# Kernel optimization log

Hardware: AMD Instinct MI355X
Metric: run time of the kernel (lower is better)

The kernel has to match this reference:

```python
import jax, jax.numpy as jnp
import numpy as np

# Config matching YoloLayer(anchor_mask=[0,1,2], num_classes=80,
#                           anchors=[116,90,156,198,373,326], num_anchors=3)
B, H, W = 32, 76, 76
NUM_CLASSES = 80
NUM_ANCHORS = 3
ANCHORS = [116.0, 90.0, 156.0, 198.0, 373.0, 326.0]
STRIDE = 32.0
C = (5 + NUM_CLASSES) * NUM_ANCHORS  # 255


def setup_inputs() -> dict:
    key = jax.random.key(0)
    output = jax.random.normal(key, (B, C, H, W), dtype=jnp.float32)
    # conf threshold (self.thresh / nms_thresh in the original forward)
    nms_thresh = jnp.float32(0.6)
    return {"output": output, "nms_thresh": nms_thresh}


def reference(output, nms_thresh):
    """Vectorized, jit-able version of get_region_boxes.

    Instead of Python-loop box lists (data-dependent shape), returns:
      boxes: [B, A, H*W, 7] = (bcx/w, bcy/h, bw/w, bh/h, det_conf,
                               cls_max_conf, cls_max_id)
      keep:  [B, A, H*W] bool mask, det_conf > thresh (only_objectness=1)
    Same math as the original decode + threshold filter.
    """
    b, _, h, w = output.shape
    na, nc = NUM_ANCHORS, NUM_CLASSES
    # masked anchors divided by stride, as in YoloLayer.forward
    anch = jnp.asarray(ANCHORS, dtype=jnp.float32).reshape(na, 2) / STRIDE

    # channel layout is (anchor, 5+nc) per the original view()
    o = output.reshape(b, na, 5 + nc, h * w)  # [B, A, 85, HW]

    # grid offsets flattened in row-major (cy, cx) order, matching ind = cy*w+cx
    gx = jnp.tile(jnp.arange(w, dtype=output.dtype), h)     # [HW]
    gy = jnp.repeat(jnp.arange(h, dtype=output.dtype), w)   # [HW]

    xs = (jax.nn.sigmoid(o[:, :, 0]) + gx) / w               # [B, A, HW]
    ys = (jax.nn.sigmoid(o[:, :, 1]) + gy) / h
    ws = jnp.exp(o[:, :, 2]) * anch[None, :, 0, None] / w
    hs = jnp.exp(o[:, :, 3]) * anch[None, :, 1, None] / h
    det_confs = jax.nn.sigmoid(o[:, :, 4])                   # [B, A, HW]

    cls_confs = jax.nn.softmax(o[:, :, 5:], axis=2)          # [B, A, NC, HW]
    cls_max_confs = jnp.max(cls_confs, axis=2)               # [B, A, HW]
    cls_max_ids = jnp.argmax(cls_confs, axis=2)              # [B, A, HW]

    boxes = jnp.stack(
        [xs, ys, ws, hs, det_confs, cls_max_confs,
         cls_max_ids.astype(output.dtype)],
        axis=-1,
    )  # [B, A, HW, 7]
    keep = det_confs > nms_thresh  # only_objectness=1 path
    return boxes, keep
```

## Files before the change

kernel.cpp:

```cpp
#include <hip/hip_runtime.h>
#include <math.h>


namespace {
constexpr int kB   = 32;
constexpr int kA   = 3;
constexpr int kNC  = 80;
constexpr int kH   = 76;
constexpr int kW   = 76;
constexpr int kHW  = kH * kW;
constexpr int kCPA = 5 + kNC;
constexpr int kTot = kB * kA * kHW;
}

__global__ __launch_bounds__(256)
void yolo_decode_kernel(const float* __restrict__ in,
                        const float* __restrict__ thrp,
                        float* __restrict__ out)
{
    const int t = blockIdx.x * 256 + threadIdx.x;
    if (t >= kTot) return;

    const float thresh = thrp[0];

    const int hw = t % kHW;
    const int ba = t / kHW;
    const int a  = ba % kA;

    const float* __restrict__ base = in + (size_t)ba * kCPA * kHW + (size_t)hw;

    const float x0 = base[0 * kHW];
    const float x1 = base[1 * kHW];
    const float x2 = base[2 * kHW];
    const float x3 = base[3 * kHW];
    const float x4 = base[4 * kHW];

    float c[kNC];
    const float* __restrict__ cbase = base + 5 * kHW;
#pragma unroll
    for (int k = 0; k < kNC; ++k) c[k] = cbase[(size_t)k * kHW];

    float m = c[0];
#pragma unroll
    for (int k = 1; k < kNC; ++k) m = fmaxf(m, c[k]);

    float s    = 0.0f;
    float emax = -1.0f;
    int   id   = 0;
#pragma unroll
    for (int k = 0; k < kNC; ++k) {
        const float e = expf(c[k] - m);
        s += e;
        if (e > emax) { emax = e; id = k; }
    }
    const float cls_conf = emax / s;

    const int gx = hw % kW;
    const int gy = hw / kW;

    const float anchw[kA] = {116.0f / 32.0f, 156.0f / 32.0f, 373.0f / 32.0f};
    const float anchh[kA] = { 90.0f / 32.0f, 198.0f / 32.0f, 326.0f / 32.0f};

    constexpr float invW = 1.0f / (float)kW;
    constexpr float invH = 1.0f / (float)kH;

    const float sig0 = 1.0f / (1.0f + expf(-x0));
    const float sig1 = 1.0f / (1.0f + expf(-x1));
    const float det  = 1.0f / (1.0f + expf(-x4));

    const float xs = (sig0 + (float)gx) * invW;
    const float ys = (sig1 + (float)gy) * invH;
    const float ws = expf(x2) * anchw[a] * invW;
    const float hs = expf(x3) * anchh[a] * invH;

    float* __restrict__ bp = out + (size_t)t * 7;
    bp[0] = xs;
    bp[1] = ys;
    bp[2] = ws;
    bp[3] = hs;
    bp[4] = det;
    bp[5] = cls_conf;
    bp[6] = (float)id;

    out[(size_t)kTot * 7 + t] = (det > thresh) ? 1.0f : 0.0f;
}

extern "C" void kernel_launch(void* const* d_in, const int* in_sizes, int n_in,
                              void* d_out, int out_size, void* d_ws, size_t ws_size,
                              hipStream_t stream) {
    (void)in_sizes; (void)n_in; (void)d_ws; (void)ws_size; (void)out_size;
    const float* in   = (const float*)d_in[0];
    const float* thrp = (const float*)d_in[1];
    float* out        = (float*)d_out;

    constexpr int kBlock = 256;
    constexpr int kGrid  = (kTot + kBlock - 1) / kBlock;
    yolo_decode_kernel<<<kGrid, kBlock, 0, stream>>>(in, thrp, out);
}
```

Measured before the change: 266.1 us.

## Process four pixels per thread with float4 loads/stores and single-pass softmax

```diff
diff --git a/kernel.cpp b/kernel.cpp
--- a/kernel.cpp
+++ b/kernel.cpp
@@ -9,80 +9,104 @@
 constexpr int kH   = 76;
 constexpr int kW   = 76;
 constexpr int kHW  = kH * kW;
+constexpr int kQ   = kHW / 4;
 constexpr int kCPA = 5 + kNC;
 constexpr int kTot = kB * kA * kHW;
+constexpr int kT4  = kB * kA * kQ;
 }
 
+__device__ __forceinline__ float sigm(float x) { return 1.0f / (1.0f + expf(-x)); }
+
 __global__ __launch_bounds__(256)
-void yolo_decode_kernel(const float* __restrict__ in,
-                        const float* __restrict__ thrp,
-                        float* __restrict__ out)
+void yolo_decode4(const float* __restrict__ in,
+                  const float* __restrict__ thrp,
+                  float* __restrict__ out)
 {
     const int t = blockIdx.x * 256 + threadIdx.x;
-    if (t >= kTot) return;
+    if (t >= kT4) return;
 
     const float thresh = thrp[0];
 
-    const int hw = t % kHW;
-    const int ba = t / kHW;
+    const int q  = t % kQ;
+    const int ba = t / kQ;
     const int a  = ba % kA;
 
-    const float* __restrict__ base = in + (size_t)ba * kCPA * kHW + (size_t)hw;
+    const float4* __restrict__ base4 =
+        reinterpret_cast<const float4*>(in + (size_t)ba * kCPA * kHW) + q;
 
-    const float x0 = base[0 * kHW];
-    const float x1 = base[1 * kHW];
-    const float x2 = base[2 * kHW];
-    const float x3 = base[3 * kHW];
-    const float x4 = base[4 * kHW];
+    const float4 cx = base4[0 * kQ];
+    const float4 cy = base4[1 * kQ];
+    const float4 cw = base4[2 * kQ];
+    const float4 ch = base4[3 * kQ];
+    const float4 co = base4[4 * kQ];
 
-    float c[kNC];
-    const float* __restrict__ cbase = base + 5 * kHW;
-#pragma unroll
-    for (int k = 0; k < kNC; ++k) c[k] = cbase[(size_t)k * kHW];
+    float s0 = 0.f, s1 = 0.f, s2 = 0.f, s3 = 0.f;
+    float e0 = -1.f, e1 = -1.f, e2 = -1.f, e3 = -1.f;
+    int   i0 = 0, i1 = 0, i2 = 0, i3 = 0;
+#pragma unroll 10
+    for (int k = 0; k < kNC; ++k) {
+        const float4 c = base4[(size_t)(5 + k) * kQ];
+        const float a0 = expf(c.x);
+        const float a1 = expf(c.y);
+        const float a2 = expf(c.z);
+        const float a3 = expf(c.w);
+        s0 += a0; s1 += a1; s2 += a2; s3 += a3;
+        if (a0 > e0) { e0 = a0; i0 = k; }
+        if (a1 > e1) { e1 = a1; i1 = k; }
+        if (a2 > e2) { e2 = a2; i2 = k; }
+        if (a3 > e3) { e3 = a3; i3 = k; }
+    }
+    const float cc0 = e0 / s0, cc1 = e1 / s1, cc2 = e2 / s2, cc3 = e3 / s3;
 
-    float m = c[0];
-#pragma unroll
-    for (int k = 1; k < kNC; ++k) m = fmaxf(m, c[k]);
+    const int hw  = q * 4;
+    const int gxb = hw % kW;
+    const int gy  = hw / kW;
 
-    float s    = 0.0f;
-    float emax = -1.0f;
-    int   id   = 0;
-#pragma unroll
-    for (int k = 0; k < kNC; ++k) {
-        const float e = expf(c[k] - m);
-        s += e;
-        if (e > emax) { emax = e; id = k; }
-    }
-    const float cls_conf = emax / s;
-
-    const int gx = hw % kW;
-    const int gy = hw / kW;
-
-    const float anchw[kA] = {116.0f / 32.0f, 156.0f / 32.0f, 373.0f / 32.0f};
-    const float anchh[kA] = { 90.0f / 32.0f, 198.0f / 32.0f, 326.0f / 32.0f};
+    const float aw = (a == 0) ? (116.0f / 32.0f) : (a == 1) ? (156.0f / 32.0f) : (373.0f / 32.0f);
+    const float ah = (a == 0) ? ( 90.0f / 32.0f) : (a == 1) ? (198.0f / 32.0f) : (326.0f / 32.0f);
 
     constexpr float invW = 1.0f / (float)kW;
     constexpr float invH = 1.0f / (float)kH;
 
-    const float sig0 = 1.0f / (1.0f + expf(-x0));
-    const float sig1 = 1.0f / (1.0f + expf(-x1));
-    const float det  = 1.0f / (1.0f + expf(-x4));
+    const float ysv = (sigm(cy.x) + (float)gy) * invH;
+    const float ys0 = ysv, ys1 = (sigm(cy.y) + (float)gy) * invH,
+                ys2 = (sigm(cy.z) + (float)gy) * invH,
+                ys3 = (sigm(cy.w) + (float)gy) * invH;
+    (void)ysv;
 
-    const float xs = (sig0 + (float)gx) * invW;
-    const float ys = (sig1 + (float)gy) * invH;
-    const float ws = expf(x2) * anchw[a] * invW;
-    const float hs = expf(x3) * anchh[a] * invH;
+    const float xs0 = (sigm(cx.x) + (float)(gxb + 0)) * invW;
+    const float xs1 = (sigm(cx.y) + (float)(gxb + 1)) * invW;
+    const float xs2 = (sigm(cx.z) + (float)(gxb + 2)) * invW;
+    const float xs3 = (sigm(cx.w) + (float)(gxb + 3)) * invW;
 
-    float* __restrict__ bp = out + (size_t)t * 7;
-    bp[0] = xs;
-    bp[1] = ys;
-    bp[2] = ws;
-    bp[3] = hs;
-    bp[4] = det;
-    bp[5] = cls_conf;
-    bp[6] = (float)id;
+    const float ws0 = expf(cw.x) * aw * invW;
+    const float ws1 = expf(cw.y) * aw * invW;
+    const float ws2 = expf(cw.z) * aw * invW;
+    const float ws3 = expf(cw.w) * aw * invW;
 
-    out[(size_t)kTot * 7 + t] = (det > thresh) ? 1.0f : 0.0f;
+    const float hs0 = expf(ch.x) * ah * invH;
+    const float hs1 = expf(ch.y) * ah * invH;
+    const float hs2 = expf(ch.z) * ah * invH;
+    const float hs3 = expf(ch.w) * ah * invH;
+
+    const float dt0 = sigm(co.x), dt1 = sigm(co.y), dt2 = sigm(co.z), dt3 = sigm(co.w);
+
+    const float id0 = (float)i0, id1 = (float)i1, id2 = (float)i2, id3 = (float)i3;
+
+    float4* __restrict__ bp = reinterpret_cast<float4*>(out + (size_t)t * 28);
+    bp[0] = make_float4(xs0, ys0, ws0, hs0);
+    bp[1] = make_float4(dt0, cc0, id0, xs1);
+    bp[2] = make_float4(ys1, ws1, hs1, dt1);
+    bp[3] = make_float4(cc1, id1, xs2, ys2);
+    bp[4] = make_float4(ws2, hs2, dt2, cc2);
+    bp[5] = make_float4(id2, xs3, ys3, ws3);
+    bp[6] = make_float4(hs3, dt3, cc3, id3);
+
+    float4* __restrict__ kp = reinterpret_cast<float4*>(out + (size_t)kTot * 7 + (size_t)t * 4);
+    *kp = make_float4(dt0 > thresh ? 1.f : 0.f,
+                      dt1 > thresh ? 1.f : 0.f,
+                      dt2 > thresh ? 1.f : 0.f,
+                      dt3 > thresh ? 1.f : 0.f);
 }
 
 extern "C" void kernel_launch(void* const* d_in, const int* in_sizes, int n_in,
@@ -94,6 +118,6 @@
     float* out        = (float*)d_out;
 
     constexpr int kBlock = 256;
-    constexpr int kGrid  = (kTot + kBlock - 1) / kBlock;
-    yolo_decode_kernel<<<kGrid, kBlock, 0, stream>>>(in, thrp, out);
+    constexpr int kGrid  = (kT4 + kBlock - 1) / kBlock;
+    yolo_decode4<<<kGrid, kBlock, 0, stream>>>(in, thrp, out);
 }
```

Measured after the change: 274.6 us. 1.03x slower.
